# Kernel optimization log

Measured on AMD Instinct MI355X. Metric: run time of the kernel, lower is better.

## Reference

```python
import jax, jax.numpy as jnp
import numpy as np
from jax import lax
from math import sqrt

POLE = sqrt(3.0) - 2.0                       # cubic B-spline pole
GAIN = (1.0 - POLE) * (1.0 - 1.0 / POLE)     # = 6.0
UPSAMPLING_FACTOR = 2


def _cubic_spline_1d(t):
    a = jnp.abs(t)
    out = (2.0 / 3.0 + (0.5 * a - 1.0) * a ** 2) * (a < 1)
    out = out + (-(a - 2.0) ** 3 / 6.0) * ((a >= 1) & (a < 2))
    return out


def _bspline_kernel(f):
    is_odd = f % 2
    k = 4 * f - is_odd
    start = (1 + is_odd) / (2 * f) - 2.0
    pts = jnp.arange(k, dtype=jnp.float32) * (1.0 / f) + start
    return _cubic_spline_1d(pts)


def _prefilter_1d(x, axis):
    """Causal + anticausal recursive cubic-spline coefficient filter along `axis`."""
    n = x.shape[axis]
    if n == 1:
        return x
    p = POLE
    xm = jnp.moveaxis(x * GAIN, axis, 0)  # (n, ...)
    i = np.arange(n)
    pows = jnp.asarray(p ** i + p ** (2 * n - 1 - i), dtype=x.dtype)
    # causal boundary condition (mirror)
    c0 = jnp.tensordot(pows, xm, axes=(0, 0)) * (p / (1.0 - p ** (2 * n))) + xm[0]

    def causal(carry, xi):
        y = xi + p * carry
        return y, y

    _, ys = lax.scan(causal, c0, xm[1:])
    cm = jnp.concatenate([c0[None], ys], axis=0)
    # anticausal boundary condition
    last = cm[-1] * (p / (p - 1.0))

    def anti(carry, ci):
        y = p * (carry - ci)
        return y, y

    _, ys2 = lax.scan(anti, last, cm[:-1], reverse=True)
    out = jnp.concatenate([ys2, last[None]], axis=0)
    return jnp.moveaxis(out, 0, axis)


def _upsample_1d(x, axis, kernel, f):
    """Strided transposed conv along `axis` with replicate padding of 2 (per-channel)."""
    dim_size = x.shape[axis]
    xm = jnp.moveaxis(x, axis, -1)
    lead = xm.shape[:-1]
    x3 = xm.reshape(-1, 1, dim_size)
    x3 = jnp.pad(x3, ((0, 0), (0, 0), (2, 2)), mode='edge')
    k = kernel.shape[0]
    implicit_padding = 7 * f // 2
    pad = k - 1 - implicit_padding  # conv_transpose == lhs-dilated correlation w/ flipped kernel
    out = lax.conv_general_dilated(
        x3,
        kernel[::-1][None, None, :],
        window_strides=(1,),
        padding=[(pad, pad)],
        lhs_dilation=(f,),
        dimension_numbers=('NCH', 'OIH', 'NCH'),
    )
    out = out.reshape(lead + (out.shape[-1],))
    return jnp.moveaxis(out, -1, axis)


def setup_inputs() -> dict:
    key = jax.random.key(0)
    volume = jax.random.normal(key, (2, 3, 96, 96, 96), dtype=jnp.float32)
    return {"volume": volume}


def reference(volume):
    f = UPSAMPLING_FACTOR
    kernel = _bspline_kernel(f).astype(volume.dtype)
    first_spatial_dim = min(volume.ndim - 1, 2)
    x = volume
    for axis in range(first_spatial_dim, volume.ndim):
        x = _prefilter_1d(x, axis)
    for axis in range(first_spatial_dim, volume.ndim):
        x = _upsample_1d(x, axis, kernel, f)
    return x
```

## Files before the change

kernel.cpp:

```cpp
#include <hip/hip_runtime.h>


#define TAPS 28
#define CHUNK 12
#define WIN (CHUNK + TAPS - 1)

__device__ double g_Wd[96 * 96];
__device__ float g_Mb[192 * TAPS];
__device__ float g_bufA[6 * 96 * 96 * 192];
__device__ float g_bufB[6 * 96 * 192 * 192];

__device__ __forceinline__ int clamp96(int j) { return j < 0 ? 0 : (j > 95 ? 95 : j); }

__global__ void compute_Wd_kernel(double* __restrict__ Wd) {
    int j = threadIdx.x;
    if (j >= 96) return;
    const double p = -0.26794919243112270647253365849413;
    double c[96];
    double pj = 1.0;
    for (int t = 0; t < j; ++t) pj *= p;
    double p191j = 1.0;
    for (int t = 0; t < 191 - j; ++t) p191j *= p;
    double p2n = 1.0;
    for (int t = 0; t < 192; ++t) p2n *= p;
    double K = p / (1.0 - p2n);
    double cur = 6.0 * K * (pj + p191j) + (j == 0 ? 6.0 : 0.0);
    c[0] = cur;
    for (int i = 1; i < 96; ++i) {
        cur = (i == j ? 6.0 : 0.0) + p * cur;
        c[i] = cur;
    }
    double nxt = cur * (p / (p - 1.0));
    Wd[95 * 96 + j] = nxt;
    for (int i = 94; i >= 0; --i) {
        nxt = p * (nxt - c[i]);
        Wd[i * 96 + j] = nxt;
    }
}

__global__ void compute_M_kernel(const double* __restrict__ Wd, float* __restrict__ Mb) {
    int i = threadIdx.x;
    if (i >= 192) return;
    const double cw[8] = {1.0 / 384.0, 121.0 / 384.0, 235.0 / 384.0, 27.0 / 384.0,
                          27.0 / 384.0, 235.0 / 384.0, 121.0 / 384.0, 1.0 / 384.0};
    int ph = i & 1;
    int c = i >> 1;
    for (int t = 0; t < TAPS; ++t) {
        int j = c - 13 + t;
        double m = 0.0;
        if (j >= 0 && j < 96) {
            for (int tt = 0; tt < 4; ++tt) {
                int k = c + ph - 2 + tt;
                k = k < 0 ? 0 : (k > 95 ? 95 : k);
                m += cw[ph * 4 + tt] * Wd[k * 96 + j];
            }
        }
        Mb[i * TAPS + t] = (float)m;
    }
}

__global__ __launch_bounds__(512) void pass_z(const float* __restrict__ in,
                                              float* __restrict__ out,
                                              const float* __restrict__ Mb) {
    __shared__ float s_in[64 * 97];
    __shared__ float s_out[64 * 193];
    float w0[TAPS], w1[TAPS];
#pragma unroll
    for (int t = 0; t < TAPS; ++t) {
        w0[t] = Mb[96 * TAPS + t];
        w1[t] = Mb[97 * TAPS + t];
    }
    size_t base = (size_t)blockIdx.x * 64;
    const float* src = in + base * 96;
    int tid = threadIdx.x;
    for (int k = tid; k < 64 * 96; k += 512)
        s_in[(k / 96) * 97 + (k % 96)] = src[k];
    __syncthreads();

    int lane = tid & 63;
    int wave = tid >> 6;
    int c0 = wave * CHUNK;
    const float* xl = s_in + lane * 97;
    float* op = s_out + lane * 193 + 2 * c0;
    float win[WIN];
#pragma unroll
    for (int k = 0; k < WIN; ++k) win[k] = xl[clamp96(c0 - 13 + k)];

    if (c0 >= 12 && c0 + CHUNK <= 84) {
#pragma unroll
        for (int mi = 0; mi < CHUNK; ++mi) {
            float a0 = 0.f, a1 = 0.f;
#pragma unroll
            for (int t = 0; t < TAPS; ++t) {
                float xv = win[mi + t];
                a0 = fmaf(w0[t], xv, a0);
                a1 = fmaf(w1[t], xv, a1);
            }
            op[2 * mi] = a0;
            op[2 * mi + 1] = a1;
        }
    } else {
#pragma unroll
        for (int mi = 0; mi < CHUNK; ++mi) {
            int m = c0 + mi;
            int wb = __builtin_amdgcn_readfirstlane(m * 2 * TAPS);
            const float* wr = Mb + wb;
            float a0 = 0.f, a1 = 0.f;
#pragma unroll
            for (int t = 0; t < TAPS; ++t) {
                float xv = win[mi + t];
                a0 = fmaf(wr[t], xv, a0);
                a1 = fmaf(wr[TAPS + t], xv, a1);
            }
            op[2 * mi] = a0;
            op[2 * mi + 1] = a1;
        }
    }
    __syncthreads();
    float* dst = out + base * 192;
    for (int k = tid; k < 64 * 192; k += 512)
        dst[k] = s_out[(k / 192) * 193 + (k % 192)];
}

template <int INNER>
__global__ __launch_bounds__(256) void pass_staged(const float* __restrict__ in,
                                                   float* __restrict__ out,
                                                   const float* __restrict__ Mb) {
    constexpr int CT = INNER / 64;
    __shared__ float s[96 * 64];
    int tid = threadIdx.x;
    int ct = blockIdx.x % CT;
    int o = blockIdx.x / CT;
    const float* src = in + (size_t)o * 96 * INNER + (size_t)ct * 64;
    float* dst = out + (size_t)o * 192 * INNER + (size_t)ct * 64;

#pragma unroll
    for (int it = 0; it < 6; ++it) {
        int k = tid + it * 256;
        int row = k >> 4;
        int c4 = k & 15;
        float4 v = *(const float4*)(src + (size_t)row * INNER + c4 * 4);
        *(float4*)(&s[row * 64 + c4 * 4]) = v;
    }
    __syncthreads();

    int col = tid & 63;
    int cq = tid >> 6;
    int c0 = cq * 24;

    float win[51];
#pragma unroll
    for (int k = 0; k < 51; ++k) win[k] = s[clamp96(c0 - 13 + k) * 64 + col];

    if (cq == 1 || cq == 2) {
        float w0[TAPS], w1[TAPS];
#pragma unroll
        for (int t = 0; t < TAPS; ++t) {
            w0[t] = Mb[96 * TAPS + t];
            w1[t] = Mb[97 * TAPS + t];
        }
#pragma unroll
        for (int mi = 0; mi < 24; ++mi) {
            float a0 = 0.f, a1 = 0.f;
#pragma unroll
            for (int t = 0; t < TAPS; ++t) {
                float xv = win[mi + t];
                a0 = fmaf(w0[t], xv, a0);
                a1 = fmaf(w1[t], xv, a1);
            }
            int m = c0 + mi;
            dst[(size_t)(2 * m) * INNER + col] = a0;
            dst[(size_t)(2 * m + 1) * INNER + col] = a1;
        }
    } else {
#pragma unroll
        for (int mi = 0; mi < 24; ++mi) {
            int m = c0 + mi;
            int wb = __builtin_amdgcn_readfirstlane(m * 2 * TAPS);
            const float* wr = Mb + wb;
            float a0 = 0.f, a1 = 0.f;
#pragma unroll
            for (int t = 0; t < TAPS; ++t) {
                float xv = win[mi + t];
                a0 = fmaf(wr[t], xv, a0);
                a1 = fmaf(wr[TAPS + t], xv, a1);
            }
            dst[(size_t)(2 * m) * INNER + col] = a0;
            dst[(size_t)(2 * m + 1) * INNER + col] = a1;
        }
    }
}

extern "C" void kernel_launch(void* const* d_in, const int* in_sizes, int n_in,
                              void* d_out, int out_size, void* d_ws, size_t ws_size,
                              hipStream_t stream) {
    const float* x = (const float*)d_in[0];
    float* out = (float*)d_out;
    double* Wd;
    float *Mb, *bufA, *bufB;
    hipGetSymbolAddress((void**)&Wd, HIP_SYMBOL(g_Wd));
    hipGetSymbolAddress((void**)&Mb, HIP_SYMBOL(g_Mb));
    hipGetSymbolAddress((void**)&bufA, HIP_SYMBOL(g_bufA));
    hipGetSymbolAddress((void**)&bufB, HIP_SYMBOL(g_bufB));

    compute_Wd_kernel<<<1, 96, 0, stream>>>(Wd);
    compute_M_kernel<<<1, 192, 0, stream>>>(Wd, Mb);

    pass_z<<<864, 512, 0, stream>>>(x, bufA, Mb);
    pass_staged<192><<<1728, 256, 0, stream>>>(bufA, bufB, Mb);
    pass_staged<36864><<<3456, 256, 0, stream>>>(bufB, out, Mb);
}
```

Before: 332.0 us.

## Fuse three separable upsample passes into one cooperative persistent kernel

Merges the z, y and x passes into a single persistent cooperative kernel that runs each stage as a loop over work units, with grid-wide syncs between stages and a three-launch fallback. The y/x passes now use 512-thread blocks with 12 outputs per wave instead of 256 threads with 24. The z pass loads and stores through float4. The aim is to remove launch gaps and tail effects between passes and to improve occupancy. The cost is grid.sync overhead, and the launch bounds of (512,4) may squeeze registers for the unrolled 28-tap windows.

```diff
diff --git a/kernel.cpp b/kernel.cpp
--- a/kernel.cpp
+++ b/kernel.cpp
@@ -1,14 +1,15 @@
 #include <hip/hip_runtime.h>
-
+#include <hip/hip_cooperative_groups.h>
+
+
+namespace cg = cooperative_groups;
 
 #define TAPS 28
-#define CHUNK 12
-#define WIN (CHUNK + TAPS - 1)
 
 __device__ double g_Wd[96 * 96];
-__device__ float g_Mb[192 * TAPS];
-__device__ float g_bufA[6 * 96 * 96 * 192];
-__device__ float g_bufB[6 * 96 * 192 * 192];
+__device__ alignas(16) float g_Mb[192 * TAPS];
+__device__ alignas(16) float g_bufA[6 * 96 * 96 * 192];
+__device__ alignas(16) float g_bufB[6 * 96 * 192 * 192];
 
 __device__ __forceinline__ int clamp96(int j) { return j < 0 ? 0 : (j > 95 ? 95 : j); }
 
@@ -59,36 +60,36 @@
     }
 }
 
-__global__ __launch_bounds__(512) void pass_z(const float* __restrict__ in,
-                                              float* __restrict__ out,
-                                              const float* __restrict__ Mb) {
-    __shared__ float s_in[64 * 97];
-    __shared__ float s_out[64 * 193];
-    float w0[TAPS], w1[TAPS];
-#pragma unroll
-    for (int t = 0; t < TAPS; ++t) {
-        w0[t] = Mb[96 * TAPS + t];
-        w1[t] = Mb[97 * TAPS + t];
-    }
-    size_t base = (size_t)blockIdx.x * 64;
-    const float* src = in + base * 96;
+
+__device__ __forceinline__ void z_unit(int u, const float* __restrict__ in,
+                                       float* __restrict__ sIn ,
+                                       float* __restrict__ sOut ) {
     int tid = threadIdx.x;
-    for (int k = tid; k < 64 * 96; k += 512)
-        s_in[(k / 96) * 97 + (k % 96)] = src[k];
-    __syncthreads();
-
-    int lane = tid & 63;
-    int wave = tid >> 6;
-    int c0 = wave * CHUNK;
-    const float* xl = s_in + lane * 97;
-    float* op = s_out + lane * 193 + 2 * c0;
-    float win[WIN];
-#pragma unroll
-    for (int k = 0; k < WIN; ++k) win[k] = xl[clamp96(c0 - 13 + k)];
-
-    if (c0 >= 12 && c0 + CHUNK <= 84) {
-#pragma unroll
-        for (int mi = 0; mi < CHUNK; ++mi) {
+    size_t base = (size_t)u * 64;
+    const float4* src4 = (const float4*)(in + base * 96);
+#pragma unroll
+    for (int i = 0; i < 3; ++i) {
+        int k4 = tid + i * 512;
+        int row = k4 / 24;
+        int c = (k4 % 24) * 4;
+        float4 v = src4[k4];
+        float* p = sIn + row * 97 + c;
+        p[0] = v.x; p[1] = v.y; p[2] = v.z; p[3] = v.w;
+    }
+    __syncthreads();
+    int lane = tid & 63, wave = tid >> 6;
+    int c0 = wave * 12;
+    const float* xl = sIn + lane * 97;
+    float* op = sOut + lane * 193 + 2 * c0;
+    float win[39];
+#pragma unroll
+    for (int k = 0; k < 39; ++k) win[k] = xl[clamp96(c0 - 13 + k)];
+    if (wave >= 1 && wave <= 6) {
+        float w0[TAPS], w1[TAPS];
+#pragma unroll
+        for (int t = 0; t < TAPS; ++t) { w0[t] = g_Mb[96 * TAPS + t]; w1[t] = g_Mb[97 * TAPS + t]; }
+#pragma unroll
+        for (int mi = 0; mi < 12; ++mi) {
             float a0 = 0.f, a1 = 0.f;
 #pragma unroll
             for (int t = 0; t < TAPS; ++t) {
@@ -101,10 +102,10 @@
         }
     } else {
 #pragma unroll
-        for (int mi = 0; mi < CHUNK; ++mi) {
+        for (int mi = 0; mi < 12; ++mi) {
             int m = c0 + mi;
             int wb = __builtin_amdgcn_readfirstlane(m * 2 * TAPS);
-            const float* wr = Mb + wb;
+            const float* wr = g_Mb + wb;
             float a0 = 0.f, a1 = 0.f;
 #pragma unroll
             for (int t = 0; t < TAPS; ++t) {
@@ -117,50 +118,46 @@
         }
     }
     __syncthreads();
-    float* dst = out + base * 192;
-    for (int k = tid; k < 64 * 192; k += 512)
-        dst[k] = s_out[(k / 192) * 193 + (k % 192)];
-}
-
-template <int INNER>
-__global__ __launch_bounds__(256) void pass_staged(const float* __restrict__ in,
-                                                   float* __restrict__ out,
-                                                   const float* __restrict__ Mb) {
-    constexpr int CT = INNER / 64;
-    __shared__ float s[96 * 64];
+    float4* dst4 = (float4*)(g_bufA + base * 192);
+#pragma unroll
+    for (int i = 0; i < 6; ++i) {
+        int k4 = tid + i * 512;
+        int row = k4 / 48;
+        int c = (k4 % 48) * 4;
+        const float* p = sOut + row * 193 + c;
+        dst4[k4] = make_float4(p[0], p[1], p[2], p[3]);
+    }
+}
+
+template <int INNER, int CT>
+__device__ __forceinline__ void yx_unit(int u, const float* __restrict__ inb,
+                                        float* __restrict__ outb,
+                                        float* __restrict__ sY ) {
     int tid = threadIdx.x;
-    int ct = blockIdx.x % CT;
-    int o = blockIdx.x / CT;
-    const float* src = in + (size_t)o * 96 * INNER + (size_t)ct * 64;
-    float* dst = out + (size_t)o * 192 * INNER + (size_t)ct * 64;
-
-#pragma unroll
-    for (int it = 0; it < 6; ++it) {
-        int k = tid + it * 256;
-        int row = k >> 4;
-        int c4 = k & 15;
-        float4 v = *(const float4*)(src + (size_t)row * INNER + c4 * 4);
-        *(float4*)(&s[row * 64 + c4 * 4]) = v;
-    }
-    __syncthreads();
-
-    int col = tid & 63;
-    int cq = tid >> 6;
-    int c0 = cq * 24;
-
-    float win[51];
-#pragma unroll
-    for (int k = 0; k < 51; ++k) win[k] = s[clamp96(c0 - 13 + k) * 64 + col];
-
-    if (cq == 1 || cq == 2) {
+    int ct = u % CT;
+    int o = u / CT;
+    const float* src = inb + (size_t)o * 96 * INNER + (size_t)ct * 64;
+    float* dst = outb + (size_t)o * 192 * INNER + (size_t)ct * 64;
+#pragma unroll
+    for (int i = 0; i < 3; ++i) {
+        int k4 = tid + i * 512;
+        int row = k4 >> 4;
+        int c4 = k4 & 15;
+        float4 v = ((const float4*)(src + (size_t)row * INNER))[c4];
+        ((float4*)(sY + row * 64))[c4] = v;
+    }
+    __syncthreads();
+    int lane = tid & 63, wave = tid >> 6;
+    int c0 = wave * 12;
+    float win[39];
+#pragma unroll
+    for (int k = 0; k < 39; ++k) win[k] = sY[clamp96(c0 - 13 + k) * 64 + lane];
+    if (wave >= 1 && wave <= 6) {
         float w0[TAPS], w1[TAPS];
 #pragma unroll
-        for (int t = 0; t < TAPS; ++t) {
-            w0[t] = Mb[96 * TAPS + t];
-            w1[t] = Mb[97 * TAPS + t];
-        }
-#pragma unroll
-        for (int mi = 0; mi < 24; ++mi) {
+        for (int t = 0; t < TAPS; ++t) { w0[t] = g_Mb[96 * TAPS + t]; w1[t] = g_Mb[97 * TAPS + t]; }
+#pragma unroll
+        for (int mi = 0; mi < 12; ++mi) {
             float a0 = 0.f, a1 = 0.f;
 #pragma unroll
             for (int t = 0; t < TAPS; ++t) {
@@ -169,15 +166,15 @@
                 a1 = fmaf(w1[t], xv, a1);
             }
             int m = c0 + mi;
-            dst[(size_t)(2 * m) * INNER + col] = a0;
-            dst[(size_t)(2 * m + 1) * INNER + col] = a1;
+            dst[(size_t)(2 * m) * INNER + lane] = a0;
+            dst[(size_t)(2 * m + 1) * INNER + lane] = a1;
         }
     } else {
 #pragma unroll
-        for (int mi = 0; mi < 24; ++mi) {
+        for (int mi = 0; mi < 12; ++mi) {
             int m = c0 + mi;
             int wb = __builtin_amdgcn_readfirstlane(m * 2 * TAPS);
-            const float* wr = Mb + wb;
+            const float* wr = g_Mb + wb;
             float a0 = 0.f, a1 = 0.f;
 #pragma unroll
             for (int t = 0; t < TAPS; ++t) {
@@ -185,10 +182,37 @@
                 a0 = fmaf(wr[t], xv, a0);
                 a1 = fmaf(wr[TAPS + t], xv, a1);
             }
-            dst[(size_t)(2 * m) * INNER + col] = a0;
-            dst[(size_t)(2 * m + 1) * INNER + col] = a1;
-        }
-    }
+            dst[(size_t)(2 * m) * INNER + lane] = a0;
+            dst[(size_t)(2 * m + 1) * INNER + lane] = a1;
+        }
+    }
+    __syncthreads();
+}
+
+__global__ __launch_bounds__(512, 4) void fused_zyx(const float* __restrict__ in,
+                                                    float* __restrict__ out) {
+    __shared__ alignas(16) float sIn[64 * 97];
+    __shared__ alignas(16) float sOut[64 * 193];
+    cg::grid_group grid = cg::this_grid();
+    for (int u = blockIdx.x; u < 864; u += gridDim.x) z_unit(u, in, sIn, sOut);
+    grid.sync();
+    for (int u = blockIdx.x; u < 576 * 3; u += gridDim.x) yx_unit<192, 3>(u, g_bufA, g_bufB, sIn);
+    grid.sync();
+    for (int u = blockIdx.x; u < 6 * 576; u += gridDim.x) yx_unit<36864, 576>(u, g_bufB, out, sIn);
+}
+
+__global__ __launch_bounds__(512) void zk(const float* __restrict__ in) {
+    __shared__ alignas(16) float sIn[64 * 97];
+    __shared__ alignas(16) float sOut[64 * 193];
+    z_unit(blockIdx.x, in, sIn, sOut);
+}
+__global__ __launch_bounds__(512) void yk() {
+    __shared__ alignas(16) float sY[96 * 64];
+    yx_unit<192, 3>(blockIdx.x, g_bufA, g_bufB, sY);
+}
+__global__ __launch_bounds__(512) void xk(float* __restrict__ out) {
+    __shared__ alignas(16) float sY[96 * 64];
+    yx_unit<36864, 576>(blockIdx.x, g_bufB, out, sY);
 }
 
 extern "C" void kernel_launch(void* const* d_in, const int* in_sizes, int n_in,
@@ -197,16 +221,28 @@
     const float* x = (const float*)d_in[0];
     float* out = (float*)d_out;
     double* Wd;
-    float *Mb, *bufA, *bufB;
+    float* Mb;
     hipGetSymbolAddress((void**)&Wd, HIP_SYMBOL(g_Wd));
     hipGetSymbolAddress((void**)&Mb, HIP_SYMBOL(g_Mb));
-    hipGetSymbolAddress((void**)&bufA, HIP_SYMBOL(g_bufA));
-    hipGetSymbolAddress((void**)&bufB, HIP_SYMBOL(g_bufB));
 
     compute_Wd_kernel<<<1, 96, 0, stream>>>(Wd);
     compute_M_kernel<<<1, 192, 0, stream>>>(Wd, Mb);
 
-    pass_z<<<864, 512, 0, stream>>>(x, bufA, Mb);
-    pass_staged<192><<<1728, 256, 0, stream>>>(bufA, bufB, Mb);
-    pass_staged<36864><<<3456, 256, 0, stream>>>(bufB, out, Mb);
-}
+    int occ = 0;
+    hipError_t oe = hipOccupancyMaxActiveBlocksPerMultiprocessor(
+        &occ, reinterpret_cast<const void*>(fused_zyx), 512, 0);
+    bool done = false;
+    if (oe == hipSuccess && occ > 0) {
+        int grid = occ * 256;
+        if (grid > 3456) grid = 3456;
+        void* args[] = {(void*)&x, (void*)&out};
+        if (hipLaunchCooperativeKernel(reinterpret_cast<const void*>(fused_zyx),
+                                       dim3(grid), dim3(512), args, 0, stream) == hipSuccess)
+            done = true;
+    }
+    if (!done) {
+        zk<<<864, 512, 0, stream>>>(x);
+        yk<<<1728, 512, 0, stream>>>();
+        xk<<<3456, 512, 0, stream>>>(out);
+    }
+}
```

Measured after the change: 774.9 us. 133% more time.
